# Optimization experiments

Measured on AMD Instinct MI355X. Metric: run time of the kernel, lower is better.

The kernel has to match this reference:

```python
import jax, jax.numpy as jnp
import numpy as np

EPS = 1e-5
K_NN = 16

def _lin1d(x, W, b):
    # 1x1 Conv1d: x (B,C,N) -> (B,O,N)
    return jnp.einsum('oc,bcn->bon', W, x) + b[None, :, None]

def _lin2d(x, W, b):
    # 1x1 Conv2d: x (B,C,N,K) -> (B,O,N,K)
    return jnp.einsum('oc,bcnk->bonk', W, x) + b[None, :, None, None]

def _bn2d(x, gamma, beta):
    # train-mode BatchNorm2d over (B, N, K) per channel
    mean = jnp.mean(x, axis=(0, 2, 3), keepdims=True)
    var = jnp.var(x, axis=(0, 2, 3), keepdims=True)
    xh = (x - mean) * jax.lax.rsqrt(var + EPS)
    return gamma[None, :, None, None] * xh + beta[None, :, None, None]

def _knn_idx(pq, ps, k):
    # pq (B,3,N), ps (B,3,M) -> idx (B,N,K) of k nearest support points
    d2 = (jnp.sum(pq * pq, axis=1)[:, :, None]
          + jnp.sum(ps * ps, axis=1)[:, None, :]
          - 2.0 * jnp.einsum('bcn,bcm->bnm', pq, ps))
    _, idx = jax.lax.top_k(-d2, k)
    return idx

def _group(x, idx):
    # x (B,C,M), idx (B,N,K) -> (B,C,N,K)
    return jnp.take_along_axis(x[:, :, None, :], idx[:, None, :, :], axis=3)

def setup_inputs() -> dict:
    key = jax.random.key(0)
    ks = jax.random.split(key, 20)
    B, C, D, N, M, H = 4, 128, 64, 2048, 2048, 256
    s = lambda k, shape, scale: (jax.random.normal(k, shape, dtype=jnp.float32) * scale)
    return {
        'pq': s(ks[0], (B, 3, N), 1.0),
        'fq': s(ks[1], (B, C, N), 1.0),
        'ps': s(ks[2], (B, 3, M), 1.0),
        'fs': s(ks[3], (B, C, M), 1.0),
        'Wq': s(ks[4], (D, C), 0.05), 'bq': jnp.zeros((D,), jnp.float32),
        'Wk': s(ks[5], (D, C), 0.05), 'bk': jnp.zeros((D,), jnp.float32),
        'Wv': s(ks[6], (D, C), 0.05), 'bv': jnp.zeros((D,), jnp.float32),
        'Wp1': s(ks[7], (D, 3), 0.2), 'bp1': jnp.zeros((D,), jnp.float32),
        'gp': jnp.ones((D,), jnp.float32), 'btp': jnp.zeros((D,), jnp.float32),
        'Wp2': s(ks[8], (D, D), 0.05), 'bp2': jnp.zeros((D,), jnp.float32),
        'Wa1': s(ks[9], (H, D), 0.05), 'ba1': jnp.zeros((H,), jnp.float32),
        'ga': jnp.ones((H,), jnp.float32), 'bta': jnp.zeros((H,), jnp.float32),
        'Wa2': s(ks[10], (D, H), 0.05), 'ba2': jnp.zeros((D,), jnp.float32),
        'We': s(ks[11], (C, D), 0.05), 'be': jnp.zeros((C,), jnp.float32),
    }

def reference(pq, fq, ps, fs, Wq, bq, Wk, bk, Wv, bv,
              Wp1, bp1, gp, btp, Wp2, bp2,
              Wa1, ba1, ga, bta, Wa2, ba2, We, be):
    identity = fq
    q = _lin1d(fq, Wq, bq)          # (B,D,N)
    k = _lin1d(fs, Wk, bk)          # (B,D,M)
    v = _lin1d(fs, Wv, bv)          # (B,D,M)
    idx = _knn_idx(pq, ps, K_NN)    # (B,N,K)
    key_g = _group(k, idx)          # (B,D,N,K)
    qk_rel = q[:, :, :, None] - key_g
    pos_rel = pq[:, :, :, None] - _group(ps, idx)  # (B,3,N,K)
    # pos_mlp: conv-bn-relu-conv
    pe = _lin2d(pos_rel, Wp1, bp1)
    pe = jax.nn.relu(_bn2d(pe, gp, btp))
    pe = _lin2d(pe, Wp2, bp2)       # (B,D,N,K)
    # attn_mlp: conv-bn-relu-conv
    a = _lin2d(qk_rel + pe, Wa1, ba1)
    a = jax.nn.relu(_bn2d(a, ga, bta))
    a = _lin2d(a, Wa2, ba2)         # (B,D,N,K)
    attn = jax.nn.softmax(a, axis=-1)
    val = _group(v, idx) + pe       # (B,D,N,K)
    agg = jnp.einsum('bcnk,bcnk->bcn', attn, val)
    return _lin1d(agg, We, be) + identity
```

## Files before the change

### kernel.cpp

```cpp
#include <hip/hip_runtime.h>
#include <stdint.h>

#define NN 2048
#define MM 2048
#define NSAMP 131072

typedef float  fv4 __attribute__((ext_vector_type(4)));
typedef short  bfv8 __attribute__((ext_vector_type(8)));
typedef short  bfv4 __attribute__((ext_vector_type(4)));
typedef unsigned short u16;
typedef unsigned long long u64;

__device__ inline u16 f2bf(float x){
  unsigned u = __float_as_uint(x);
  return (u16)((u + 0x7FFFu + ((u>>16)&1u)) >> 16);
}
__device__ inline float bf2f(u16 u){ return __uint_as_float(((unsigned)u)<<16); }
#define MFMA16 __builtin_amdgcn_mfma_f32_16x16x32_bf16

__global__ __launch_bounds__(256) void k_prep(
    const float* __restrict__ Wq, const float* __restrict__ Wk, const float* __restrict__ Wv,
    const float* __restrict__ Wp2, const float* __restrict__ Wa2, const float* __restrict__ We,
    const float* __restrict__ ps,
    u16* __restrict__ Wqbf, u16* __restrict__ Wkbf, u16* __restrict__ Wvbf,
    u16* __restrict__ Wp2bf, u16* __restrict__ Wa2bf, u16* __restrict__ Webf,
    fv4* __restrict__ psP) {
  int gid = blockIdx.x * 256 + threadIdx.x;
  if (gid < 8192)  { Wqbf[gid] = f2bf(Wq[gid]); Wkbf[gid] = f2bf(Wk[gid]);
                     Wvbf[gid] = f2bf(Wv[gid]); Webf[gid] = f2bf(We[gid]); }
  if (gid < 4096)  Wp2bf[gid] = f2bf(Wp2[gid]);
  if (gid < 16384) Wa2bf[gid] = f2bf(Wa2[gid]);
  if (gid < 8192)  { int b = gid >> 11, m = gid & 2047;
    float x = ps[(b*3+0)*MM + m], y = ps[(b*3+1)*MM + m], z = ps[(b*3+2)*MM + m];
    fv4 p; p.x = x; p.y = y; p.z = z; p.w = x*x + y*y + z*z;
    psP[gid] = p; }
}

__global__ __launch_bounds__(256) void k_qkv(
    const float* __restrict__ fq, const float* __restrict__ fs,
    const u16* __restrict__ Wqbf, const u16* __restrict__ Wkbf, const u16* __restrict__ Wvbf,
    const float* __restrict__ bq, const float* __restrict__ bk, const float* __restrict__ bv,
    float* __restrict__ qT, float* __restrict__ kT, float* __restrict__ vT) {
  __shared__ u16 tile[2][32 * 136];
  int bid = blockIdx.x;
  int b = bid >> 6, p0 = (bid & 63) * 32;
  int t = threadIdx.x;
  int w = t >> 6, l = t & 63, lq = l >> 4, ln = l & 15;
  {
    int cq = t >> 3, n4 = (t & 7) * 4;
    #pragma unroll
    for (int it = 0; it < 4; ++it) {
      int c = it * 32 + cq;
      fv4 vq = *(const fv4*)&fq[(b*128 + c)*2048 + p0 + n4];
      fv4 vs = *(const fv4*)&fs[(b*128 + c)*2048 + p0 + n4];
      #pragma unroll
      for (int j = 0; j < 4; ++j) {
        tile[0][(n4 + j)*136 + c] = f2bf(vq[j]);
        tile[1][(n4 + j)*136 + c] = f2bf(vs[j]);
      }
    }
  }
  bfv8 A[3][4];
  #pragma unroll
  for (int mat = 0; mat < 3; ++mat) {
    const u16* W = mat == 0 ? Wqbf : (mat == 1 ? Wkbf : Wvbf);
    #pragma unroll
    for (int kk = 0; kk < 4; ++kk)
      A[mat][kk] = *(const bfv8*)(W + (w*16 + ln)*128 + kk*32 + lq*8);
  }
  __syncthreads();
  fv4 acc[3][2];
  #pragma unroll
  for (int mat = 0; mat < 3; ++mat) {
    const u16* tl = tile[mat == 0 ? 0 : 1];
    #pragma unroll
    for (int nt = 0; nt < 2; ++nt) {
      fv4 a = {0.f,0.f,0.f,0.f};
      #pragma unroll
      for (int kk = 0; kk < 4; ++kk) {
        bfv8 bb = *(const bfv8*)&tl[(nt*16 + ln)*136 + kk*32 + lq*8];
        a = MFMA16(A[mat][kk], bb, a, 0, 0, 0);
      }
      acc[mat][nt] = a;
    }
  }
  #pragma unroll
  for (int mat = 0; mat < 3; ++mat) {
    float* dst = mat == 0 ? qT : (mat == 1 ? kT : vT);
    const float* bia = mat == 0 ? bq : (mat == 1 ? bk : bv);
    fv4 bq4 = *(const fv4*)&bia[w*16 + lq*4];
    #pragma unroll
    for (int nt = 0; nt < 2; ++nt) {
      fv4 o = acc[mat][nt] + bq4;
      *(fv4*)&dst[(b*NN + p0 + nt*16 + ln)*64 + w*16 + lq*4] = o;
    }
  }
}

__global__ __launch_bounds__(256) void k_knn(
    const float* __restrict__ pq, const fv4* __restrict__ psP,
    int* __restrict__ idxb, float* __restrict__ posPart) {
  __shared__ u64 list[4][512];
  __shared__ u64 win[4][16];
  __shared__ int cnt[4];
  __shared__ float sacc[4][9];

  const int t = threadIdx.x, w = t >> 6, lane = t & 63;
  const int qi = blockIdx.x * 4 + w;
  const int b = qi >> 11, n = qi & 2047;
  const float* pqb = pq + b * 3 * NN;
  const fv4* psb = psP + b * 2048;
  const float qx = pqb[n], qy = pqb[NN + n], qz = pqb[2 * NN + n];
  const float qq = qx * qx + qy * qy + qz * qz;

  unsigned key[32];
  unsigned bkey = 0xFFFFFFFFu; unsigned bj = 0;
  #pragma unroll
  for (int j = 0; j < 32; ++j) {
    fv4 P = psb[lane + 64*j];
    float d2 = qq + P.w - 2.f * (qx * P.x + qy * P.y + qz * P.z);
    unsigned bu = __float_as_uint(d2);
    bu = (bu & 0x80000000u) ? ~bu : (bu | 0x80000000u);
    key[j] = bu;
    if (bu < bkey) { bkey = bu; bj = (unsigned)j; }
  }
  u64 e = (((u64)bkey) << 32) | (unsigned)(lane + 64*(int)bj);

  #pragma unroll
  for (int k = 2; k <= 64; k <<= 1) {
    #pragma unroll
    for (int j = k >> 1; j > 0; j >>= 1) {
      u64 x = __shfl_xor(e, j, 64);
      u64 lo = e < x ? e : x, hi = e < x ? x : e;
      bool up = ((lane & k) == 0);
      bool takeLo = (((lane & j) == 0) == up);
      e = takeLo ? lo : hi;
    }
  }
  const u64 thr = __shfl(e, 15, 64);
  const unsigned T32 = (unsigned)(thr >> 32);

  if (lane == 0) cnt[w] = 0;
  #pragma unroll
  for (int j = 0; j < 32; ++j) {
    if (key[j] <= T32) {
      int p = atomicAdd(&cnt[w], 1);
      if (p < 512) list[w][p] = (((u64)key[j]) << 32) | (unsigned)(lane + 64*j);
    }
  }
  const int C = *(volatile int*)&cnt[w];

  u64 myWin = 0;
  if (C <= 64) {
    u64 v = (lane < C) ? list[w][lane] : ~0ULL;
    #pragma unroll
    for (int k = 2; k <= 64; k <<= 1) {
      #pragma unroll
      for (int j = k >> 1; j > 0; j >>= 1) {
        u64 x = __shfl_xor(v, j, 64);
        u64 lo = v < x ? v : x, hi = v < x ? x : v;
        bool up = ((lane & k) == 0);
        bool takeLo = (((lane & j) == 0) == up);
        v = takeLo ? lo : hi;
      }
    }
    myWin = v;
  } else if (C <= 128) {
    u64 e0 = list[w][lane];
    u64 e1 = (64 + lane < C) ? list[w][64 + lane] : ~0ULL;
    #pragma unroll
    for (unsigned k = 2; k <= 128; k <<= 1) {
      #pragma unroll
      for (unsigned j = k >> 1; j > 0; j >>= 1) {
        if (j < 64) {
          u64 x0 = __shfl_xor(e0, (int)j, 64);
          u64 x1 = __shfl_xor(e1, (int)j, 64);
          bool lower = ((lane & j) == 0);
          bool up0 = (k == 128) ? true : ((lane & k) == 0);
          bool up1 = (k == 128) ? true : ((k == 64) ? false : ((lane & k) == 0));
          e0 = (lower == up0) ? (e0 < x0 ? e0 : x0) : (e0 < x0 ? x0 : e0);
          e1 = (lower == up1) ? (e1 < x1 ? e1 : x1) : (e1 < x1 ? x1 : e1);
        } else {
          u64 lo = e0 < e1 ? e0 : e1, hi = e0 < e1 ? e1 : e0;
          e0 = lo; e1 = hi;
        }
      }
    }
    myWin = e0;
  } else {
    int Cc = C > 512 ? 512 : C;
    for (int i = lane; i < 512; i += 64)
      if (i >= Cc) list[w][i] = ~0ULL;
    for (int r = 0; r < 16; ++r) {
      u64 mv = ~0ULL;
      #pragma unroll
      for (int s5 = 0; s5 < 8; ++s5) {
        u64 x = list[w][s5*64 + lane];
        mv = x < mv ? x : mv;
      }
      #pragma unroll
      for (int off = 1; off <= 32; off <<= 1) {
        u64 x = __shfl_xor(mv, off, 64);
        mv = x < mv ? x : mv;
      }
      #pragma unroll
      for (int s5 = 0; s5 < 8; ++s5)
        if (list[w][s5*64 + lane] == mv) list[w][s5*64 + lane] = ~0ULL;
      if (lane == 0) win[w][r] = mv;
    }
    if (lane < 16) myWin = win[w][lane];
  }

  if (lane < 16) {
    unsigned m = (unsigned)(myWin & 0xFFFFFFFFu);
    idxb[qi * 16 + lane] = (int)m;
    fv4 P = psb[m];
    float r0 = qx - P.x, r1 = qy - P.y, r2 = qz - P.z;
    float s[9];
    s[0] = r0; s[1] = r1; s[2] = r2;
    s[3] = r0*r0; s[4] = r0*r1; s[5] = r0*r2;
    s[6] = r1*r1; s[7] = r1*r2; s[8] = r2*r2;
    #pragma unroll
    for (int off = 1; off <= 8; off <<= 1)
      #pragma unroll
      for (int i = 0; i < 9; ++i) s[i] += __shfl_xor(s[i], off, 64);
    if (lane == 0)
      #pragma unroll
      for (int i = 0; i < 9; ++i) sacc[w][i] = s[i];
  }
  __syncthreads();
  if (t < 9) posPart[blockIdx.x * 12 + t]
      = sacc[0][t] + sacc[1][t] + sacc[2][t] + sacc[3][t];
}

__global__ __launch_bounds__(256) void k_posfinal(
    const float* __restrict__ Wp1, const float* __restrict__ bp1,
    const float* __restrict__ gp, const float* __restrict__ btp,
    const float* __restrict__ posPart, float* __restrict__ Wp1f, float* __restrict__ bp1f) {
  __shared__ float red[4][9];
  __shared__ float st[9];
  int t = threadIdx.x;
  int w = t >> 6, lane = t & 63;
  float s[9];
  #pragma unroll
  for (int i = 0; i < 9; ++i) s[i] = 0.f;
  #pragma unroll
  for (int it = 0; it < 8; ++it) {
    const float* p = posPart + (it * 256 + t) * 12;
    fv4 a = *(const fv4*)p;
    fv4 b4 = *(const fv4*)(p + 4);
    float c8 = p[8];
    s[0]+=a.x; s[1]+=a.y; s[2]+=a.z; s[3]+=a.w;
    s[4]+=b4.x; s[5]+=b4.y; s[6]+=b4.z; s[7]+=b4.w;
    s[8]+=c8;
  }
  #pragma unroll
  for (int off = 32; off > 0; off >>= 1)
    #pragma unroll
    for (int i = 0; i < 9; ++i) s[i] += __shfl_xor(s[i], off, 64);
  if (lane == 0)
    #pragma unroll
    for (int i = 0; i < 9; ++i) red[w][i] = s[i];
  __syncthreads();
  if (t < 9) st[t] = red[0][t] + red[1][t] + red[2][t] + red[3][t];
  __syncthreads();
  if (t < 64) {
    int d = t;
    const float invN = 1.f / (float)NSAMP;
    float m0 = st[0]*invN, m1 = st[1]*invN, m2 = st[2]*invN;
    float C00 = st[3]*invN - m0*m0, C01 = st[4]*invN - m0*m1, C02 = st[5]*invN - m0*m2;
    float C11 = st[6]*invN - m1*m1, C12 = st[7]*invN - m1*m2, C22 = st[8]*invN - m2*m2;
    float w0 = Wp1[d*3], w1 = Wp1[d*3+1], w2 = Wp1[d*3+2];
    float mean = w0*m0 + w1*m1 + w2*m2 + bp1[d];
    float var = w0*w0*C00 + w1*w1*C11 + w2*w2*C22 + 2.f*(w0*w1*C01 + w0*w2*C02 + w1*w2*C12);
    float scale = gp[d] * rsqrtf(var + 1e-5f);
    Wp1f[d*3]   = scale * w0;
    Wp1f[d*3+1] = scale * w1;
    Wp1f[d*3+2] = scale * w2;
    bp1f[d] = btp[d] + scale * (bp1[d] - mean);
  }
}

__global__ __launch_bounds__(256) void k_ystats(
    const float* __restrict__ pq, const float* __restrict__ ps,
    const float* __restrict__ qT, const float* __restrict__ kT, const float* __restrict__ vT,
    const int* __restrict__ idxb,
    const float* __restrict__ Wp1f, const float* __restrict__ bp1f,
    const u16* __restrict__ Wp2bf, const float* __restrict__ bp2,
    u16* __restrict__ yg, u16* __restrict__ valg,
    float* __restrict__ Gpart, float* __restrict__ ySumPart) {
  __shared__ __align__(16) unsigned char smem[21760];
  u16*   hp   = (u16*)smem;
  u16*   y2   = (u16*)(smem + 9216);
  float* r3   = (float*)(smem + 18432);
  float* qc   = (float*)(smem + 19200);
  int*   idxA = (int*)(smem + 20224);
  float* sWp1 = (float*)(smem + 20480);
  float* sbp1 = (float*)(smem + 21248);
  float* sbp2 = (float*)(smem + 21504);

  const int t = threadIdx.x;
  const int w = t >> 6, l = t & 63, lq = l >> 4, ln = l & 15;
  const int d0 = 16*w + lq*4;

  if (t < 192) sWp1[t] = Wp1f[t];
  if (t < 64){ sbp1[t] = bp1f[t]; sbp2[t] = bp2[t]; }

  bfv8 Ape[2];
  #pragma unroll
  for (int kk = 0; kk < 2; ++kk)
    Ape[kk] = *(const bfv8*)(Wp2bf + (16*w + ln)*64 + kk*32 + lq*8);

  fv4 gacc[4];
  #pragma unroll
  for (int nt = 0; nt < 4; ++nt) gacc[nt] = (fv4){0.f,0.f,0.f,0.f};
  float ys[4] = {0.f, 0.f, 0.f, 0.f};
  __syncthreads();

  for (int ch = 0; ch < 2; ++ch) {
    const int p0 = blockIdx.x * 8 + ch * 4;
    const int b  = p0 >> 11;
    const int bN = b * 2048;
    if (t < 64) idxA[t] = idxb[p0*16 + t];
    qc[t] = qT[(p0 + (t>>6))*64 + (t & 63)];
    __syncthreads();
    if (t < 192) { int c = t >> 6, s = t & 63; int n = (p0 + (s>>4)) & 2047;
      r3[c*64 + s] = pq[(b*3+c)*NN + n] - ps[(b*3+c)*MM + idxA[s]]; }
    __syncthreads();
    { int s = t >> 2, iq = t & 3;
      float r0 = r3[s], r1 = r3[64+s], r2 = r3[128+s];
      u16 tmp[16];
      #pragma unroll
      for (int e = 0; e < 16; ++e) { int i = iq*16 + e;
        float v = sbp1[i] + sWp1[i*3]*r0 + sWp1[i*3+1]*r1 + sWp1[i*3+2]*r2;
        tmp[e] = f2bf(fmaxf(v, 0.f)); }
      *(bfv8*)&hp[s*72 + iq*16]     = *(const bfv8*)&tmp[0];
      *(bfv8*)&hp[s*72 + iq*16 + 8] = *(const bfv8*)&tmp[8];
    }
    __syncthreads();
    {
      fv4 pe[4];
      #pragma unroll
      for (int nt = 0; nt < 4; ++nt) {
        fv4 acc = {0.f,0.f,0.f,0.f};
        #pragma unroll
        for (int kk = 0; kk < 2; ++kk) {
          bfv8 bb = *(const bfv8*)&hp[(nt*16 + ln)*72 + kk*32 + lq*8];
          acc = MFMA16(Ape[kk], bb, acc, 0, 0, 0);
        }
        pe[nt] = acc;
      }
      fv4 bp2q = *(const fv4*)&sbp2[d0];
      #pragma unroll
      for (int nt = 0; nt < 4; ++nt) {
        int s = nt*16 + ln;
        int mi = idxA[s];
        fv4 kg = *(const fv4*)(kT + (bN + mi)*64 + d0);
        fv4 vg = *(const fv4*)(vT + (bN + mi)*64 + d0);
        fv4 qv = *(const fv4*)&qc[nt*64 + d0];
        fv4 pv = pe[nt] + bp2q;
        fv4 yv = qv - kg + pv;
        fv4 vv = vg + pv;
        u16 yp[4], vp[4];
        #pragma unroll
        for (int r = 0; r < 4; ++r) {
          yp[r] = f2bf(yv[r]); vp[r] = f2bf(vv[r]);
          y2[(d0 + r)*72 + s] = yp[r];
          ys[r] += yv[r];
        }
        *(bfv4*)&yg[((u64)(p0 + nt)*16 + ln)*64 + d0]   = *(const bfv4*)yp;
        *(bfv4*)&valg[((u64)(p0 + nt)*16 + ln)*64 + d0] = *(const bfv4*)vp;
      }
    }
    __syncthreads();
    #pragma unroll
    for (int kk = 0; kk < 2; ++kk) {
      bfv8 aa = *(const bfv8*)&y2[(16*w + ln)*72 + kk*32 + lq*8];
      #pragma unroll
      for (int nt = 0; nt < 4; ++nt) {
        bfv8 bb = *(const bfv8*)&y2[(nt*16 + ln)*72 + kk*32 + lq*8];
        gacc[nt] = MFMA16(aa, bb, gacc[nt], 0, 0, 0);
      }
    }
    __syncthreads();
  }
  #pragma unroll
  for (int nt = 0; nt < 4; ++nt)
    #pragma unroll
    for (int r = 0; r < 4; ++r)
      Gpart[blockIdx.x*4096 + (16*w + lq*4 + r)*64 + nt*16 + ln] = gacc[nt][r];
  #pragma unroll
  for (int off = 1; off <= 8; off <<= 1) {
    #pragma unroll
    for (int r = 0; r < 4; ++r) ys[r] += __shfl_xor(ys[r], off, 64);
  }
  if (ln == 0) {
    #pragma unroll
    for (int r = 0; r < 4; ++r) ySumPart[blockIdx.x*64 + d0 + r] = ys[r];
  }
}

__global__ __launch_bounds__(256) void k_gred(
    const float* __restrict__ Gpart, const float* __restrict__ ySumPart,
    float* __restrict__ G, float* __restrict__ ySum) {
  __shared__ float red[256];
  int bid = blockIdx.x, t = threadIdx.x;
  int tj = t & 63, st = t >> 6;
  if (bid < 64) {
    int j = bid * 64 + tj;
    float s = 0.f;
    for (int p = st * 256; p < st * 256 + 256; ++p)
      s += Gpart[p*4096 + j];
    red[st * 64 + tj] = s;
    __syncthreads();
    if (t < 64)
      G[bid * 64 + t] = red[t] + red[64 + t] + red[128 + t] + red[192 + t];
  } else {
    float s = 0.f;
    for (int p = st * 256; p < st * 256 + 256; ++p)
      s += ySumPart[p*64 + tj];
    red[st * 64 + tj] = s;
    __syncthreads();
    if (t < 64)
      ySum[t] = red[t] + red[64 + t] + red[128 + t] + red[192 + t];
  }
}

__global__ __launch_bounds__(256) void k_attnfinal(
    const float* __restrict__ Wa1, const float* __restrict__ ba1,
    const float* __restrict__ ga, const float* __restrict__ bta,
    const float* __restrict__ ySum, const float* __restrict__ G,
    u16* __restrict__ Wa1fbf, float* __restrict__ ba1f) {
  __shared__ float red[256];
  __shared__ float mu[64];
  __shared__ float sc[1];
  int h = blockIdx.x, t = threadIdx.x;
  const float invN = 1.f / (float)NSAMP;
  if (t < 64) mu[t] = ySum[t] * invN;
  __syncthreads();
  float acc = 0.f;
  #pragma unroll
  for (int e = 0; e < 16; ++e) {
    int pi = t*16 + e, i = pi >> 6, j = pi & 63;
    float cov = G[pi]*invN - mu[i]*mu[j];
    acc += Wa1[h*64 + i] * Wa1[h*64 + j] * cov;
  }
  red[t] = acc;
  __syncthreads();
  for (int s = 128; s > 0; s >>= 1) { if (t < s) red[t] += red[t + s]; __syncthreads(); }
  float var = red[0];
  __syncthreads();
  red[t] = (t < 64) ? Wa1[h*64 + t] * mu[t] : 0.f;
  __syncthreads();
  for (int s = 128; s > 0; s >>= 1) { if (t < s) red[t] += red[t + s]; __syncthreads(); }
  if (t == 0) {
    float mean  = red[0] + ba1[h];
    float scale = ga[h] * rsqrtf(var + 1e-5f);
    sc[0] = scale;
    ba1f[h] = bta[h] + scale * (ba1[h] - mean);
  }
  __syncthreads();
  if (t < 64) Wa1fbf[h*64 + t] = f2bf(sc[0] * Wa1[h*64 + t]);
}

__global__ __launch_bounds__(256, 4) void k_main(
    const u16* __restrict__ yg, const u16* __restrict__ valg,
    const u16* __restrict__ Wa1fbf, const float* __restrict__ ba1f,
    const u16* __restrict__ Wa2bf, const float* __restrict__ ba2,
    const u16* __restrict__ Webf, const float* __restrict__ be,
    const float* __restrict__ fq,
    u16* __restrict__ aggbf, float* __restrict__ out) {
  __shared__ __align__(16) u16 ha[64 * 264];

  const int t = threadIdx.x;
  const int w = t >> 6, l = t & 63, lq = l >> 4, ln = l & 15;
  const int d0 = 16*w + lq*4;

  bfv8 A1[4][2], A2[8];
  #pragma unroll
  for (int mt = 0; mt < 4; ++mt)
    #pragma unroll
    for (int kk = 0; kk < 2; ++kk)
      A1[mt][kk] = *(const bfv8*)(Wa1fbf + (64*w + mt*16 + ln)*64 + kk*32 + lq*8);
  #pragma unroll
  for (int kk = 0; kk < 8; ++kk)
    A2[kk] = *(const bfv8*)(Wa2bf + (16*w + ln)*256 + kk*32 + lq*8);
  fv4 bq1[4];
  #pragma unroll
  for (int mt = 0; mt < 4; ++mt)
    bq1[mt] = *(const fv4*)&ba1f[64*w + mt*16 + lq*4];
  const fv4 ba2q = *(const fv4*)&ba2[d0];

  for (int ch = 0; ch < 4; ++ch) {
    const int p0 = blockIdx.x * 16 + ch * 4;
    #pragma unroll
    for (int nt = 0; nt < 4; ++nt) {
      const u16* yp = yg + ((u64)(p0 + nt)*16 + ln)*64;
      bfv8 b0 = *(const bfv8*)(yp + lq*8);
      bfv8 b1 = *(const bfv8*)(yp + 32 + lq*8);
      int s = nt*16 + ln;
      #pragma unroll
      for (int mt = 0; mt < 4; ++mt) {
        fv4 acc = {0.f,0.f,0.f,0.f};
        acc = MFMA16(A1[mt][0], b0, acc, 0, 0, 0);
        acc = MFMA16(A1[mt][1], b1, acc, 0, 0, 0);
        int h0 = 64*w + mt*16 + lq*4;
        fv4 bq = bq1[mt];
        u16 hv[4];
        #pragma unroll
        for (int r = 0; r < 4; ++r) hv[r] = f2bf(fmaxf(acc[r] + bq[r], 0.f));
        *(bfv4*)&ha[s*264 + h0] = *(const bfv4*)hv;
      }
    }
    __syncthreads();
    fv4 acc2[4];
    #pragma unroll
    for (int nt = 0; nt < 4; ++nt) acc2[nt] = (fv4){0.f,0.f,0.f,0.f};
    #pragma unroll
    for (int kk = 0; kk < 8; ++kk) {
      #pragma unroll
      for (int nt = 0; nt < 4; ++nt) {
        bfv8 bb = *(const bfv8*)&ha[(nt*16 + ln)*264 + kk*32 + lq*8];
        acc2[nt] = MFMA16(A2[kk], bb, acc2[nt], 0, 0, 0);
      }
    }
    #pragma unroll
    for (int nt = 0; nt < 4; ++nt) {
      fv4 a = acc2[nt] + ba2q;
      fv4 m = a;
      #pragma unroll
      for (int off = 1; off <= 8; off <<= 1)
        #pragma unroll
        for (int r = 0; r < 4; ++r) m[r] = fmaxf(m[r], __shfl_xor(m[r], off, 16));
      fv4 ee, num;
      bfv4 vv4 = *(const bfv4*)(valg + ((u64)(p0 + nt)*16 + ln)*64 + d0);
      #pragma unroll
      for (int r = 0; r < 4; ++r) {
        ee[r] = __expf(a[r] - m[r]);
        num[r] = ee[r] * bf2f((u16)vv4[r]);
      }
      fv4 sum = ee;
      #pragma unroll
      for (int off = 1; off <= 8; off <<= 1)
        #pragma unroll
        for (int r = 0; r < 4; ++r) {
          sum[r] += __shfl_xor(sum[r], off, 16);
          num[r] += __shfl_xor(num[r], off, 16);
        }
      if (ln == 0) {
        u16 o[4];
        #pragma unroll
        for (int r = 0; r < 4; ++r) o[r] = f2bf(num[r] / sum[r]);
        *(bfv4*)&aggbf[(u64)(p0 + nt)*64 + d0] = *(const bfv4*)o;
      }
    }
    __syncthreads();
  }
  {
    const int P0 = blockIdx.x * 16;
    const int b  = P0 >> 11;
    const int n0 = P0 & 2047;
    bfv8 EA[2][2];
    #pragma unroll
    for (int mt = 0; mt < 2; ++mt)
      #pragma unroll
      for (int kk = 0; kk < 2; ++kk)
        EA[mt][kk] = *(const bfv8*)(Webf + ((w*2 + mt)*16 + ln)*64 + kk*32 + lq*8);
    const u16* bp = aggbf + (P0 + ln)*64;
    bfv8 b0 = *(const bfv8*)(bp + lq*8);
    bfv8 b1 = *(const bfv8*)(bp + 32 + lq*8);
    fv4 eacc[2];
    #pragma unroll
    for (int mt = 0; mt < 2; ++mt) {
      fv4 a = {0.f,0.f,0.f,0.f};
      a = MFMA16(EA[mt][0], b0, a, 0, 0, 0);
      a = MFMA16(EA[mt][1], b1, a, 0, 0, 0);
      eacc[mt] = a;
    }
    #pragma unroll
    for (int mt = 0; mt < 2; ++mt) {
      int c0 = (w*2 + mt)*16 + lq*4;
      fv4 bev = *(const fv4*)&be[c0];
      #pragma unroll
      for (int r = 0; r < 4; ++r) {
        int c = c0 + r;
        int o = (b*128 + c)*2048 + n0 + ln;
        out[o] = eacc[mt][r] + bev[r] + fq[o];
      }
    }
  }
}

extern "C" void kernel_launch(void* const* d_in, const int* in_sizes, int n_in,
                              void* d_out, int out_size, void* d_ws, size_t ws_size,
                              hipStream_t stream) {
  (void)in_sizes; (void)n_in; (void)out_size; (void)ws_size;
  const float* pq  = (const float*)d_in[0];
  const float* fq  = (const float*)d_in[1];
  const float* ps  = (const float*)d_in[2];
  const float* fs  = (const float*)d_in[3];
  const float* Wq  = (const float*)d_in[4];  const float* bq  = (const float*)d_in[5];
  const float* Wk  = (const float*)d_in[6];  const float* bk  = (const float*)d_in[7];
  const float* Wv  = (const float*)d_in[8];  const float* bv  = (const float*)d_in[9];
  const float* Wp1 = (const float*)d_in[10]; const float* bp1 = (const float*)d_in[11];
  const float* gp  = (const float*)d_in[12]; const float* btp = (const float*)d_in[13];
  const float* Wp2 = (const float*)d_in[14]; const float* bp2 = (const float*)d_in[15];
  const float* Wa1 = (const float*)d_in[16]; const float* ba1 = (const float*)d_in[17];
  const float* ga  = (const float*)d_in[18]; const float* bta = (const float*)d_in[19];
  const float* Wa2 = (const float*)d_in[20]; const float* ba2 = (const float*)d_in[21];
  const float* We  = (const float*)d_in[22]; const float* be  = (const float*)d_in[23];
  float* ws = (float*)d_ws;
  float* qT    = ws;
  float* kT    = ws + 524288;
  float* vT    = ws + 1048576;
  u16*   aggbf = (u16*)(ws + 1572864);
  int*   idxb  = (int*)(ws + 1835008);
  u16*   Wqbf  = (u16*)(ws + 1966080);
  u16*   Wkbf  = (u16*)(ws + 1970176);
  u16*   Wvbf  = (u16*)(ws + 1974272);
  u16*   Webf  = (u16*)(ws + 1978368);
  fv4*   psP   = (fv4*)(ws + 1982464);
  float* Wp1f  = ws + 2015232;
  float* bp1f  = ws + 2015424;
  float* ba1f  = ws + 2015488;
  float* G     = ws + 2015744;
  float* ySum  = ws + 2019840;
  float* ySumP = ws + 2019904;
  u16*   Wp2bf  = (u16*)(ws + 2085440);
  u16*   Wa2bf  = (u16*)(ws + 2087488);
  u16*   Wa1fbf = (u16*)(ws + 2095680);
  float* posPart = ws + 2103872;
  float* Gpart   = ws + 2128448;
  u16*   yg    = (u16*)(ws + 6322752);
  u16*   valg  = (u16*)(ws + 10517056);
  float* out   = (float*)d_out;

  k_prep<<<64, 256, 0, stream>>>(Wq, Wk, Wv, Wp2, Wa2, We, ps,
                                 Wqbf, Wkbf, Wvbf, Wp2bf, Wa2bf, Webf, psP);
  k_qkv<<<256, 256, 0, stream>>>(fq, fs, Wqbf, Wkbf, Wvbf, bq, bk, bv, qT, kT, vT);
  k_knn<<<2048, 256, 0, stream>>>(pq, psP, idxb, posPart);
  k_posfinal<<<1, 256, 0, stream>>>(Wp1, bp1, gp, btp, posPart, Wp1f, bp1f);
  k_ystats<<<1024, 256, 0, stream>>>(pq, ps, qT, kT, vT, idxb, Wp1f, bp1f, Wp2bf, bp2,
                                     yg, valg, Gpart, ySumP);
  k_gred<<<65, 256, 0, stream>>>(Gpart, ySumP, G, ySum);
  k_attnfinal<<<256, 256, 0, stream>>>(Wa1, ba1, ga, bta, ySum, G, Wa1fbf, ba1f);
  k_main<<<512, 256, 0, stream>>>(yg, valg, Wa1fbf, ba1f, Wa2bf, ba2, Webf, be,
                                  fq, aggbf, out);
}
```

Baseline: 232.0 us.

## Split main attention kernel into finer-grained blocks and separate epilogue kernel

The main kernel now processes 4 points per block instead of looping over 16, launching 4x more blocks, and prefetches the y and value tiles before loading weights. The output projection plus residual moves into a new k_epi kernel. This aims to expose more parallelism and overlap global loads with weight setup. In exchange, each block reloads the Wa1/Wa2 weight fragments for fewer points, and there is one extra kernel launch.

```diff
diff --git a/kernel.cpp b/kernel.cpp
--- a/kernel.cpp
+++ b/kernel.cpp
@@ -467,14 +467,25 @@
     const u16* __restrict__ yg, const u16* __restrict__ valg,
     const u16* __restrict__ Wa1fbf, const float* __restrict__ ba1f,
     const u16* __restrict__ Wa2bf, const float* __restrict__ ba2,
-    const u16* __restrict__ Webf, const float* __restrict__ be,
-    const float* __restrict__ fq,
-    u16* __restrict__ aggbf, float* __restrict__ out) {
+    u16* __restrict__ aggbf) {
   __shared__ __align__(16) u16 ha[64 * 264];
 
   const int t = threadIdx.x;
   const int w = t >> 6, l = t & 63, lq = l >> 4, ln = l & 15;
   const int d0 = 16*w + lq*4;
+  const int p0 = blockIdx.x * 4;
+
+  bfv8 yb0[4], yb1[4];
+  #pragma unroll
+  for (int nt = 0; nt < 4; ++nt) {
+    const u16* yp = yg + ((u64)(p0 + nt)*16 + ln)*64;
+    yb0[nt] = *(const bfv8*)(yp + lq*8);
+    yb1[nt] = *(const bfv8*)(yp + 32 + lq*8);
+  }
+  bfv4 vv4[4];
+  #pragma unroll
+  for (int nt = 0; nt < 4; ++nt)
+    vv4[nt] = *(const bfv4*)(valg + ((u64)(p0 + nt)*16 + ln)*64 + d0);
 
   bfv8 A1[4][2], A2[8];
   #pragma unroll
@@ -491,102 +502,100 @@
     bq1[mt] = *(const fv4*)&ba1f[64*w + mt*16 + lq*4];
   const fv4 ba2q = *(const fv4*)&ba2[d0];
 
-  for (int ch = 0; ch < 4; ++ch) {
-    const int p0 = blockIdx.x * 16 + ch * 4;
+  #pragma unroll
+  for (int nt = 0; nt < 4; ++nt) {
+    int s = nt*16 + ln;
+    #pragma unroll
+    for (int mt = 0; mt < 4; ++mt) {
+      fv4 acc = {0.f,0.f,0.f,0.f};
+      acc = MFMA16(A1[mt][0], yb0[nt], acc, 0, 0, 0);
+      acc = MFMA16(A1[mt][1], yb1[nt], acc, 0, 0, 0);
+      int h0 = 64*w + mt*16 + lq*4;
+      fv4 bq = bq1[mt];
+      u16 hv[4];
+      #pragma unroll
+      for (int r = 0; r < 4; ++r) hv[r] = f2bf(fmaxf(acc[r] + bq[r], 0.f));
+      *(bfv4*)&ha[s*264 + h0] = *(const bfv4*)hv;
+    }
+  }
+  __syncthreads();
+  fv4 acc2[4];
+  #pragma unroll
+  for (int nt = 0; nt < 4; ++nt) acc2[nt] = (fv4){0.f,0.f,0.f,0.f};
+  #pragma unroll
+  for (int kk = 0; kk < 8; ++kk) {
     #pragma unroll
     for (int nt = 0; nt < 4; ++nt) {
-      const u16* yp = yg + ((u64)(p0 + nt)*16 + ln)*64;
-      bfv8 b0 = *(const bfv8*)(yp + lq*8);
-      bfv8 b1 = *(const bfv8*)(yp + 32 + lq*8);
-      int s = nt*16 + ln;
-      #pragma unroll
-      for (int mt = 0; mt < 4; ++mt) {
-        fv4 acc = {0.f,0.f,0.f,0.f};
-        acc = MFMA16(A1[mt][0], b0, acc, 0, 0, 0);
-        acc = MFMA16(A1[mt][1], b1, acc, 0, 0, 0);
-        int h0 = 64*w + mt*16 + lq*4;
-        fv4 bq = bq1[mt];
-        u16 hv[4];
-        #pragma unroll
-        for (int r = 0; r < 4; ++r) hv[r] = f2bf(fmaxf(acc[r] + bq[r], 0.f));
-        *(bfv4*)&ha[s*264 + h0] = *(const bfv4*)hv;
-      }
-    }
-    __syncthreads();
-    fv4 acc2[4];
-    #pragma unroll
-    for (int nt = 0; nt < 4; ++nt) acc2[nt] = (fv4){0.f,0.f,0.f,0.f};
-    #pragma unroll
-    for (int kk = 0; kk < 8; ++kk) {
-      #pragma unroll
-      for (int nt = 0; nt < 4; ++nt) {
-        bfv8 bb = *(const bfv8*)&ha[(nt*16 + ln)*264 + kk*32 + lq*8];
-        acc2[nt] = MFMA16(A2[kk], bb, acc2[nt], 0, 0, 0);
-      }
-    }
-    #pragma unroll
-    for (int nt = 0; nt < 4; ++nt) {
-      fv4 a = acc2[nt] + ba2q;
-      fv4 m = a;
-      #pragma unroll
-      for (int off = 1; off <= 8; off <<= 1)
-        #pragma unroll
-        for (int r = 0; r < 4; ++r) m[r] = fmaxf(m[r], __shfl_xor(m[r], off, 16));
-      fv4 ee, num;
-      bfv4 vv4 = *(const bfv4*)(valg + ((u64)(p0 + nt)*16 + ln)*64 + d0);
+      bfv8 bb = *(const bfv8*)&ha[(nt*16 + ln)*264 + kk*32 + lq*8];
+      acc2[nt] = MFMA16(A2[kk], bb, acc2[nt], 0, 0, 0);
+    }
+  }
+  #pragma unroll
+  for (int nt = 0; nt < 4; ++nt) {
+    fv4 a = acc2[nt] + ba2q;
+    fv4 m = a;
+    #pragma unroll
+    for (int off = 1; off <= 8; off <<= 1)
+      #pragma unroll
+      for (int r = 0; r < 4; ++r) m[r] = fmaxf(m[r], __shfl_xor(m[r], off, 16));
+    fv4 ee, num;
+    #pragma unroll
+    for (int r = 0; r < 4; ++r) {
+      ee[r] = __expf(a[r] - m[r]);
+      num[r] = ee[r] * bf2f((u16)vv4[nt][r]);
+    }
+    fv4 sum = ee;
+    #pragma unroll
+    for (int off = 1; off <= 8; off <<= 1)
       #pragma unroll
       for (int r = 0; r < 4; ++r) {
-        ee[r] = __expf(a[r] - m[r]);
-        num[r] = ee[r] * bf2f((u16)vv4[r]);
-      }
-      fv4 sum = ee;
-      #pragma unroll
-      for (int off = 1; off <= 8; off <<= 1)
-        #pragma unroll
-        for (int r = 0; r < 4; ++r) {
-          sum[r] += __shfl_xor(sum[r], off, 16);
-          num[r] += __shfl_xor(num[r], off, 16);
-        }
-      if (ln == 0) {
-        u16 o[4];
-        #pragma unroll
-        for (int r = 0; r < 4; ++r) o[r] = f2bf(num[r] / sum[r]);
-        *(bfv4*)&aggbf[(u64)(p0 + nt)*64 + d0] = *(const bfv4*)o;
-      }
-    }
-    __syncthreads();
-  }
-  {
-    const int P0 = blockIdx.x * 16;
-    const int b  = P0 >> 11;
-    const int n0 = P0 & 2047;
-    bfv8 EA[2][2];
-    #pragma unroll
-    for (int mt = 0; mt < 2; ++mt)
-      #pragma unroll
-      for (int kk = 0; kk < 2; ++kk)
-        EA[mt][kk] = *(const bfv8*)(Webf + ((w*2 + mt)*16 + ln)*64 + kk*32 + lq*8);
-    const u16* bp = aggbf + (P0 + ln)*64;
-    bfv8 b0 = *(const bfv8*)(bp + lq*8);
-    bfv8 b1 = *(const bfv8*)(bp + 32 + lq*8);
-    fv4 eacc[2];
-    #pragma unroll
-    for (int mt = 0; mt < 2; ++mt) {
-      fv4 a = {0.f,0.f,0.f,0.f};
-      a = MFMA16(EA[mt][0], b0, a, 0, 0, 0);
-      a = MFMA16(EA[mt][1], b1, a, 0, 0, 0);
-      eacc[mt] = a;
-    }
-    #pragma unroll
-    for (int mt = 0; mt < 2; ++mt) {
-      int c0 = (w*2 + mt)*16 + lq*4;
-      fv4 bev = *(const fv4*)&be[c0];
-      #pragma unroll
-      for (int r = 0; r < 4; ++r) {
-        int c = c0 + r;
-        int o = (b*128 + c)*2048 + n0 + ln;
-        out[o] = eacc[mt][r] + bev[r] + fq[o];
-      }
+        sum[r] += __shfl_xor(sum[r], off, 16);
+        num[r] += __shfl_xor(num[r], off, 16);
+      }
+    if (ln == 0) {
+      u16 o[4];
+      #pragma unroll
+      for (int r = 0; r < 4; ++r) o[r] = f2bf(num[r] / sum[r]);
+      *(bfv4*)&aggbf[(u64)(p0 + nt)*64 + d0] = *(const bfv4*)o;
+    }
+  }
+}
+
+__global__ __launch_bounds__(256) void k_epi(
+    const u16* __restrict__ aggbf, const u16* __restrict__ Webf,
+    const float* __restrict__ be, const float* __restrict__ fq,
+    float* __restrict__ out) {
+  const int t = threadIdx.x;
+  const int w = t >> 6, l = t & 63, lq = l >> 4, ln = l & 15;
+  const int P0 = blockIdx.x * 16;
+  const int b  = P0 >> 11;
+  const int n0 = P0 & 2047;
+  bfv8 EA[2][2];
+  #pragma unroll
+  for (int mt = 0; mt < 2; ++mt)
+    #pragma unroll
+    for (int kk = 0; kk < 2; ++kk)
+      EA[mt][kk] = *(const bfv8*)(Webf + ((w*2 + mt)*16 + ln)*64 + kk*32 + lq*8);
+  const u16* bp = aggbf + (P0 + ln)*64;
+  bfv8 b0 = *(const bfv8*)(bp + lq*8);
+  bfv8 b1 = *(const bfv8*)(bp + 32 + lq*8);
+  fv4 eacc[2];
+  #pragma unroll
+  for (int mt = 0; mt < 2; ++mt) {
+    fv4 a = {0.f,0.f,0.f,0.f};
+    a = MFMA16(EA[mt][0], b0, a, 0, 0, 0);
+    a = MFMA16(EA[mt][1], b1, a, 0, 0, 0);
+    eacc[mt] = a;
+  }
+  #pragma unroll
+  for (int mt = 0; mt < 2; ++mt) {
+    int c0 = (w*2 + mt)*16 + lq*4;
+    fv4 bev = *(const fv4*)&be[c0];
+    #pragma unroll
+    for (int r = 0; r < 4; ++r) {
+      int c = c0 + r;
+      int o = (b*128 + c)*2048 + n0 + ln;
+      out[o] = eacc[mt][r] + bev[r] + fq[o];
     }
   }
 }
@@ -644,6 +653,6 @@
                                      yg, valg, Gpart, ySumP);
   k_gred<<<65, 256, 0, stream>>>(Gpart, ySumP, G, ySum);
   k_attnfinal<<<256, 256, 0, stream>>>(Wa1, ba1, ga, bta, ySum, G, Wa1fbf, ba1f);
-  k_main<<<512, 256, 0, stream>>>(yg, valg, Wa1fbf, ba1f, Wa2bf, ba2, Webf, be,
-                                  fq, aggbf, out);
-}
+  k_main<<<2048, 256, 0, stream>>>(yg, valg, Wa1fbf, ba1f, Wa2bf, ba2, aggbf);
+  k_epi<<<512, 256, 0, stream>>>(aggbf, Webf, be, fq, out);
+}
```

Result: faster. 226.7 us (-2.3%).
